# Performance work log

Measured on AMD Instinct MI355X. Metric: run time of the kernel, lower is better.

The kernel has to match this reference:

```python
import jax, jax.numpy as jnp
import numpy as np

B, S, E, H = 16, 2048, 512, 64


def setup_inputs() -> dict:
    key = jax.random.key(0)
    k1, k2, k3, k4, k5 = jax.random.split(key, 5)
    inp = {
        "input": jax.random.normal(k1, (B, S, E), dtype=jnp.float32),
        "seq_lengths": jax.random.randint(k2, (B,), 0, S).astype(jnp.int64),
        "Wq": jax.random.normal(k3, (E, H), dtype=jnp.float32) * (1.0 / np.sqrt(E)),
        "Wk": jax.random.normal(k4, (E, H), dtype=jnp.float32) * (1.0 / np.sqrt(E)),
        "Wv": jax.random.normal(k5, (E, H), dtype=jnp.float32) * (1.0 / np.sqrt(E)),
    }
    return inp


def reference(input, seq_lengths, Wq, Wk, Wv):
    # Projections (bias-free Linear): [B,S,E] @ [E,H] -> [B,S,H]
    q = input @ Wq
    k = input @ Wk
    v = input @ Wv
    Sdim = input.shape[1]
    head_size = Wk.shape[-1]
    # Padding mask: position >= seq_length -> True. Zero out q and k (NOT v),
    # exactly as the torch module does with masked_fill.
    pad = (jnp.arange(Sdim)[None, :] >= seq_lengths[:, None])[:, :, None]  # [B,S,1]
    q = jnp.where(pad, 0.0, q)
    k = jnp.where(pad, 0.0, k)
    scale = 1.0 / np.sqrt(head_size).astype(np.float32)
    # Full score matrix [B,S,S] (the memory-bound intermediate)
    scores = jnp.einsum("bsh,bth->bst", q, k) * scale
    weights = jax.nn.softmax(scores, axis=-1)
    weights = jnp.where(jnp.isnan(weights), 0.0, weights)
    out = jnp.einsum("bst,bth->bsh", weights, v)  # [B,S,H]
    return out
```

## Files before the change

kernel.cpp:

```cpp
#include <hip/hip_runtime.h>
#include <hip/hip_bf16.h>

typedef __bf16 bf16;
typedef __bf16 bf16x8 __attribute__((ext_vector_type(8)));
typedef __bf16 bf16x4 __attribute__((ext_vector_type(4)));
typedef float  f32x4  __attribute__((ext_vector_type(4)));

static constexpr int SDIM = 2048;
static constexpr int EDIM = 512;
static constexpr int HDIM = 64;

typedef __attribute__((address_space(1))) const void* gptr_t;
typedef __attribute__((address_space(3))) void*       lptr_t;

__device__ __forceinline__ void gl_lds16(const bf16* g, bf16* l) {
  __builtin_amdgcn_global_load_lds((gptr_t)g, (lptr_t)l, 16, 0, 0);
}

#if __has_builtin(__builtin_amdgcn_exp2f)
#define EXP2F(x) __builtin_amdgcn_exp2f(x)
#else
#define EXP2F(x) exp2f(x)
#endif

__device__ __forceinline__ bf16x8 pack8(f32x4 a, f32x4 b) {
  bf16x8 r;
  r[0] = (bf16)a[0]; r[1] = (bf16)a[1]; r[2] = (bf16)a[2]; r[3] = (bf16)a[3];
  r[4] = (bf16)b[0]; r[5] = (bf16)b[1]; r[6] = (bf16)b[2]; r[7] = (bf16)b[3];
  return r;
}

__global__ __launch_bounds__(256) void wt_kernel(const float* __restrict__ Wq,
                                                 const float* __restrict__ Wk,
                                                 const float* __restrict__ Wv,
                                                 bf16* __restrict__ Wt) {
  __shared__ float lds[64][65];
  const int mat = blockIdx.x >> 3;
  const int et  = blockIdx.x & 7;
  const float* W = (mat == 0) ? Wq : ((mat == 1) ? Wk : Wv);
  const float scale = (mat == 0) ? 0.18033688f : 1.0f;
  const int t  = threadIdx.x;
  const int er = t >> 2;
  const int c4 = (t & 3) * 16;
#pragma unroll
  for (int j = 0; j < 4; ++j) {
    f32x4 v = *(const f32x4*)(W + (size_t)(et * 64 + er) * HDIM + c4 + j * 4);
    lds[er][c4 + j * 4 + 0] = v[0]; lds[er][c4 + j * 4 + 1] = v[1];
    lds[er][c4 + j * 4 + 2] = v[2]; lds[er][c4 + j * 4 + 3] = v[3];
  }
  __syncthreads();
  const int h  = t >> 2;
  const int ec = (t & 3) * 16;
  bf16x8 o0, o1;
#pragma unroll
  for (int j = 0; j < 8; ++j) o0[j] = (bf16)(lds[ec + j][h] * scale);
#pragma unroll
  for (int j = 0; j < 8; ++j) o1[j] = (bf16)(lds[ec + 8 + j][h] * scale);
  bf16* dst = Wt + mat * (HDIM * EDIM) + (size_t)h * EDIM + et * 64 + ec;
  *(bf16x8*)dst = o0;
  *(bf16x8*)(dst + 8) = o1;
}

__global__ __launch_bounds__(256) void proj_kernel(const float* __restrict__ x,
                                                   const bf16* __restrict__ Wt,
                                                   const int* __restrict__ lens,
                                                   bf16* __restrict__ qo,
                                                   bf16* __restrict__ ko,
                                                   bf16* __restrict__ vT) {
  __shared__ __align__(16) bf16 wbuf[2][192 * 64];
  const int tid  = threadIdx.x;
  const int wave = tid >> 6;
  const int lane = tid & 63;
  const int quad = lane >> 4;
  const int l16  = lane & 15;
  const int rowbase = blockIdx.x * 64 + wave * 16;
  const int b = blockIdx.x >> 5;
  const float* xrow = x + (size_t)(rowbase + l16) * EDIM + quad * 8;
  const int srow   = lane >> 3;
  const int schunk = (lane & 7) ^ srow;

  #define WSTAGE(ck, buf) { _Pragma("unroll")                                  \
    for (int i6 = 0; i6 < 6; ++i6) {                                           \
      const int R0 = (wave * 6 + i6) * 8;                                      \
      gl_lds16(Wt + (size_t)(R0 + srow) * EDIM + (ck) * 64 + schunk * 8,       \
               &(buf)[R0 * 64]); } }

  f32x4 acc[3][4];
#pragma unroll
  for (int m = 0; m < 3; ++m)
#pragma unroll
    for (int nt = 0; nt < 4; ++nt) acc[m][nt] = (f32x4){0.f, 0.f, 0.f, 0.f};

  #define WCOMPUTE(buf, eo4, afrag) { _Pragma("unroll")                        \
    for (int m = 0; m < 3; ++m) { _Pragma("unroll")                            \
      for (int nt = 0; nt < 4; ++nt) {                                         \
        bf16x8 bfv = *(const bf16x8*)(&(buf)[(m * 64 + nt * 16 + l16) * 64 +   \
                                             ((((eo4) + quad) ^ (l16 & 7)) * 8)]); \
        acc[m][nt] = __builtin_amdgcn_mfma_f32_16x16x32_bf16(afrag, bfv, acc[m][nt], 0, 0, 0); } } }

  WSTAGE(0, wbuf[0]);
  f32x4 xA0 = *(const f32x4*)(xrow);
  f32x4 xB0 = *(const f32x4*)(xrow + 4);
  f32x4 xA1 = *(const f32x4*)(xrow + 32);
  f32x4 xB1 = *(const f32x4*)(xrow + 36);
#pragma unroll 2
  for (int ck = 0; ck < 8; ++ck) {
    __syncthreads();
    const int ksn = (ck < 7) ? (ck + 1) * 2 : 14;
    f32x4 nA0 = *(const f32x4*)(xrow + ksn * 32);
    f32x4 nB0 = *(const f32x4*)(xrow + ksn * 32 + 4);
    f32x4 nA1 = *(const f32x4*)(xrow + ksn * 32 + 32);
    f32x4 nB1 = *(const f32x4*)(xrow + ksn * 32 + 36);
    if (ck + 1 < 8) WSTAGE(ck + 1, wbuf[(ck + 1) & 1]);
    bf16x8 a = pack8(xA0, xB0);
    WCOMPUTE(wbuf[ck & 1], 0, a);
    a = pack8(xA1, xB1);
    WCOMPUTE(wbuf[ck & 1], 4, a);
    xA0 = nA0; xB0 = nB0; xA1 = nA1; xB1 = nB1;
  }

  int odd_or = 0;
#pragma unroll
  for (int i = 1; i < 16; i += 2) odd_or |= lens[i];
  const int len = (odd_or == 0) ? lens[2 * b] : lens[b];

#pragma unroll
  for (int nt = 0; nt < 4; ++nt) {
    const int h = nt * 16 + l16;
    bf16x4 vv;
#pragma unroll
    for (int r = 0; r < 4; ++r) {
      const int row = rowbase + quad * 4 + r;
      const int s = row & (SDIM - 1);
      const bool pad = (s >= len);
      qo[(size_t)row * HDIM + h] = (bf16)(pad ? 0.f : acc[0][nt][r]);
      ko[(size_t)row * HDIM + h] = (bf16)(pad ? 0.f : acc[1][nt][r]);
      vv[r] = (bf16)acc[2][nt][r];
    }
    *(bf16x4*)(vT + ((size_t)b * HDIM + h) * SDIM + (rowbase & (SDIM - 1)) + quad * 4) = vv;
  }
  #undef WSTAGE
  #undef WCOMPUTE
}

__global__ __launch_bounds__(256) void attn_kernel(const bf16* __restrict__ qb,
                                                   const bf16* __restrict__ kb,
                                                   const bf16* __restrict__ vT,
                                                   float* __restrict__ out) {
  __shared__ __align__(16) bf16 Kbuf[2][64 * 64];
  __shared__ __align__(16) bf16 Vbuf[2][64 * 64];
  __shared__ __align__(16) bf16 plds[4][2][16 * 64];
  const int tid  = threadIdx.x;
  const int wave = tid >> 6;
  const int lane = tid & 63;
  const int quad = lane >> 4;
  const int l16  = lane & 15;
  const int xcd = blockIdx.x & 7;
  const int jj  = blockIdx.x >> 3;
  const int b   = xcd * 2 + (jj >> 5);
  const int qbase = (jj & 31) * 64 + wave * 16;
  const bf16* q0 = qb + (size_t)b * SDIM * HDIM;
  const bf16* k0 = kb + (size_t)b * SDIM * HDIM;
  const bf16* v0 = vT + (size_t)b * HDIM * SDIM;
  const int swz = (l16 & 7) << 3;
  const int srow   = lane >> 3;
  const int schunk = (lane & 7) ^ (srow & 7);

  bf16x8 qf[2];
#pragma unroll
  for (int c = 0; c < 2; ++c)
    qf[c] = *(const bf16x8*)(q0 + (size_t)(qbase + l16) * HDIM + c * 32 + quad * 8);

  f32x4 O[4];
  float l_acc = 0.f;
#pragma unroll
  for (int ht = 0; ht < 4; ++ht) O[ht] = (f32x4){0.f, 0.f, 0.f, 0.f};
  bf16x8 vfp[4][2];

  #define STAGE(sidx, KB, VB)                                                  \
    {                                                                          \
      const int key0_ = (sidx) * 64;                                           \
      _Pragma("unroll")                                                        \
      for (int j8 = 0; j8 < 2; ++j8) {                                         \
        const int r0 = wave * 16 + j8 * 8;                                     \
        gl_lds16(k0 + (size_t)(key0_ + r0 + srow) * HDIM + schunk * 8,         \
                 &(KB)[r0 * 64]);                                              \
        gl_lds16(v0 + (size_t)(r0 + srow) * SDIM + key0_ + schunk * 8,         \
                 &(VB)[r0 * 64]);                                              \
      }                                                                        \
    }

  STAGE(0, Kbuf[0], Vbuf[0]);
#pragma unroll 2
  for (int s = 0; s < 32; ++s) {
    __syncthreads();
    if (s + 1 < 32) STAGE(s + 1, Kbuf[(s + 1) & 1], Vbuf[(s + 1) & 1]);
    const bf16* KB = Kbuf[s & 1];
    const bf16* VB = Vbuf[s & 1];
    bf16* PW = &plds[wave][s & 1][0];
    const bf16* PR = &plds[wave][(s & 1) ^ 1][0];

    bf16x8 pa[2];
    if (s) {
#pragma unroll
      for (int kc = 0; kc < 2; ++kc)
        pa[kc] = *(const bf16x8*)(&PR[l16 * 64 + (((kc * 4 + quad) << 3) ^ swz)]);
    }

    bf16x8 kf[4][2], vf[4][2];
#pragma unroll
    for (int kt = 0; kt < 4; ++kt)
#pragma unroll
      for (int c = 0; c < 2; ++c)
        kf[kt][c] = *(const bf16x8*)(&KB[(kt * 16 + l16) * 64 + (((c * 4 + quad) << 3) ^ swz)]);
#pragma unroll
    for (int ht = 0; ht < 4; ++ht)
#pragma unroll
      for (int kc = 0; kc < 2; ++kc)
        vf[ht][kc] = *(const bf16x8*)(&VB[(ht * 16 + l16) * 64 + (((kc * 4 + quad) << 3) ^ swz)]);

#pragma unroll
    for (int kt = 0; kt < 4; ++kt) {
      f32x4 st = (f32x4){0.f, 0.f, 0.f, 0.f};
      st = __builtin_amdgcn_mfma_f32_16x16x32_bf16(kf[kt][0], qf[0], st, 0, 0, 0);
      st = __builtin_amdgcn_mfma_f32_16x16x32_bf16(kf[kt][1], qf[1], st, 0, 0, 0);
      f32x4 p;
      p[0] = EXP2F(st[0]); p[1] = EXP2F(st[1]);
      p[2] = EXP2F(st[2]); p[3] = EXP2F(st[3]);
      l_acc += (p[0] + p[1]) + (p[2] + p[3]);
      bf16x4 pb;
      pb[0] = (bf16)p[0]; pb[1] = (bf16)p[1]; pb[2] = (bf16)p[2]; pb[3] = (bf16)p[3];
      const int coff = (((kt * 2 + (quad >> 1)) << 3) ^ swz) + (quad & 1) * 4;
      *(bf16x4*)(&PW[l16 * 64 + coff]) = pb;
    }

    if (s) {
#pragma unroll
      for (int ht = 0; ht < 4; ++ht) {
        O[ht] = __builtin_amdgcn_mfma_f32_16x16x32_bf16(pa[0], vfp[ht][0], O[ht], 0, 0, 0);
        O[ht] = __builtin_amdgcn_mfma_f32_16x16x32_bf16(pa[1], vfp[ht][1], O[ht], 0, 0, 0);
      }
    }
#pragma unroll
    for (int ht = 0; ht < 4; ++ht)
#pragma unroll
      for (int kc = 0; kc < 2; ++kc) vfp[ht][kc] = vf[ht][kc];
  }

  {
    bf16x8 pa[2];
    const bf16* PR = &plds[wave][1][0];
#pragma unroll
    for (int kc = 0; kc < 2; ++kc)
      pa[kc] = *(const bf16x8*)(&PR[l16 * 64 + (((kc * 4 + quad) << 3) ^ swz)]);
#pragma unroll
    for (int ht = 0; ht < 4; ++ht) {
      O[ht] = __builtin_amdgcn_mfma_f32_16x16x32_bf16(pa[0], vfp[ht][0], O[ht], 0, 0, 0);
      O[ht] = __builtin_amdgcn_mfma_f32_16x16x32_bf16(pa[1], vfp[ht][1], O[ht], 0, 0, 0);
    }
  }

  l_acc += __shfl_xor(l_acc, 16);
  l_acc += __shfl_xor(l_acc, 32);
  const float inv_own = 1.0f / l_acc;
#pragma unroll
  for (int r = 0; r < 4; ++r) {
    const float inv = __shfl(inv_own, (lane & 48) + quad * 4 + r);
    const int row = qbase + quad * 4 + r;
#pragma unroll
    for (int ht = 0; ht < 4; ++ht)
      out[((size_t)b * SDIM + row) * HDIM + ht * 16 + l16] = O[ht][r] * inv;
  }
  #undef STAGE
}

extern "C" void kernel_launch(void* const* d_in, const int* in_sizes, int n_in,
                              void* d_out, int out_size, void* d_ws, size_t ws_size,
                              hipStream_t stream) {
  (void)in_sizes; (void)n_in; (void)out_size; (void)ws_size;
  const float* x  = (const float*)d_in[0];
  const int*   sl = (const int*)d_in[1];
  const float* Wq = (const float*)d_in[2];
  const float* Wk = (const float*)d_in[3];
  const float* Wv = (const float*)d_in[4];
  float* out = (float*)d_out;

  char* ws = (char*)d_ws;
  bf16* Wt = (bf16*)(ws);
  bf16* qb = (bf16*)(ws + (256 << 10));
  bf16* kb = (bf16*)(ws + (256 << 10) + (4 << 20));
  bf16* vT = (bf16*)(ws + (256 << 10) + (8 << 20));

  wt_kernel  <<<24,  256, 0, stream>>>(Wq, Wk, Wv, Wt);
  proj_kernel<<<512, 256, 0, stream>>>(x, Wt, sl, qb, kb, vT);
  attn_kernel<<<512, 256, 0, stream>>>(qb, kb, vT, out);
}
```

Baseline: 141.3 us.

## Load V fragments directly from global into registers instead of via LDS

Removes the LDS staging buffer for V. Each wave now loads its V MFMA operand fragments straight from global memory into a double-buffered register array one step ahead, and the P·V MFMA is moved to the start of each iteration. This cuts LDS traffic and footprint, which could raise occupancy. The cost is that every wave redundantly loads the same V tile from global/L2, and register pressure rises.

```diff
diff --git a/kernel.cpp b/kernel.cpp
--- a/kernel.cpp
+++ b/kernel.cpp
@@ -148,7 +148,6 @@
                                                    const bf16* __restrict__ vT,
                                                    float* __restrict__ out) {
   __shared__ __align__(16) bf16 Kbuf[2][64 * 64];
-  __shared__ __align__(16) bf16 Vbuf[2][64 * 64];
   __shared__ __align__(16) bf16 plds[4][2][16 * 64];
   const int tid  = threadIdx.x;
   const int wave = tid >> 6;
@@ -175,9 +174,8 @@
   float l_acc = 0.f;
 #pragma unroll
   for (int ht = 0; ht < 4; ++ht) O[ht] = (f32x4){0.f, 0.f, 0.f, 0.f};
-  bf16x8 vfp[4][2];
-
-  #define STAGE(sidx, KB, VB)                                                  \
+
+  #define STAGEK(sidx, KB)                                                     \
     {                                                                          \
       const int key0_ = (sidx) * 64;                                           \
       _Pragma("unroll")                                                        \
@@ -185,39 +183,50 @@
         const int r0 = wave * 16 + j8 * 8;                                     \
         gl_lds16(k0 + (size_t)(key0_ + r0 + srow) * HDIM + schunk * 8,         \
                  &(KB)[r0 * 64]);                                              \
-        gl_lds16(v0 + (size_t)(r0 + srow) * SDIM + key0_ + schunk * 8,         \
-                 &(VB)[r0 * 64]);                                              \
       }                                                                        \
     }
 
-  STAGE(0, Kbuf[0], Vbuf[0]);
+  #define VLOAD(sidx, dst)                                                     \
+    {                                                                          \
+      const int key0_ = (sidx) * 64;                                           \
+      _Pragma("unroll")                                                        \
+      for (int ht = 0; ht < 4; ++ht)                                           \
+        _Pragma("unroll")                                                      \
+        for (int kc = 0; kc < 2; ++kc)                                         \
+          dst[ht][kc] = *(const bf16x8*)(v0 + (size_t)(ht * 16 + l16) * SDIM + \
+                                         key0_ + kc * 32 + quad * 8);          \
+    }
+
+  bf16x8 vv[2][4][2];
+  STAGEK(0, Kbuf[0]);
+  VLOAD(0, vv[0]);
 #pragma unroll 2
   for (int s = 0; s < 32; ++s) {
     __syncthreads();
-    if (s + 1 < 32) STAGE(s + 1, Kbuf[(s + 1) & 1], Vbuf[(s + 1) & 1]);
+    if (s + 1 < 32) STAGEK(s + 1, Kbuf[(s + 1) & 1]);
     const bf16* KB = Kbuf[s & 1];
-    const bf16* VB = Vbuf[s & 1];
     bf16* PW = &plds[wave][s & 1][0];
     const bf16* PR = &plds[wave][(s & 1) ^ 1][0];
 
-    bf16x8 pa[2];
     if (s) {
+      bf16x8 pa[2];
 #pragma unroll
       for (int kc = 0; kc < 2; ++kc)
         pa[kc] = *(const bf16x8*)(&PR[l16 * 64 + (((kc * 4 + quad) << 3) ^ swz)]);
-    }
-
-    bf16x8 kf[4][2], vf[4][2];
+#pragma unroll
+      for (int ht = 0; ht < 4; ++ht) {
+        O[ht] = __builtin_amdgcn_mfma_f32_16x16x32_bf16(pa[0], vv[(s - 1) & 1][ht][0], O[ht], 0, 0, 0);
+        O[ht] = __builtin_amdgcn_mfma_f32_16x16x32_bf16(pa[1], vv[(s - 1) & 1][ht][1], O[ht], 0, 0, 0);
+      }
+    }
+    if (s + 1 < 32) VLOAD(s + 1, vv[(s + 1) & 1]);
+
+    bf16x8 kf[4][2];
 #pragma unroll
     for (int kt = 0; kt < 4; ++kt)
 #pragma unroll
       for (int c = 0; c < 2; ++c)
         kf[kt][c] = *(const bf16x8*)(&KB[(kt * 16 + l16) * 64 + (((c * 4 + quad) << 3) ^ swz)]);
-#pragma unroll
-    for (int ht = 0; ht < 4; ++ht)
-#pragma unroll
-      for (int kc = 0; kc < 2; ++kc)
-        vf[ht][kc] = *(const bf16x8*)(&VB[(ht * 16 + l16) * 64 + (((kc * 4 + quad) << 3) ^ swz)]);
 
 #pragma unroll
     for (int kt = 0; kt < 4; ++kt) {
@@ -233,21 +242,10 @@
       const int coff = (((kt * 2 + (quad >> 1)) << 3) ^ swz) + (quad & 1) * 4;
       *(bf16x4*)(&PW[l16 * 64 + coff]) = pb;
     }
-
-    if (s) {
-#pragma unroll
-      for (int ht = 0; ht < 4; ++ht) {
-        O[ht] = __builtin_amdgcn_mfma_f32_16x16x32_bf16(pa[0], vfp[ht][0], O[ht], 0, 0, 0);
-        O[ht] = __builtin_amdgcn_mfma_f32_16x16x32_bf16(pa[1], vfp[ht][1], O[ht], 0, 0, 0);
-      }
-    }
-#pragma unroll
-    for (int ht = 0; ht < 4; ++ht)
-#pragma unroll
-      for (int kc = 0; kc < 2; ++kc) vfp[ht][kc] = vf[ht][kc];
   }
 
   {
+    __builtin_amdgcn_s_waitcnt(0xc07f);
     bf16x8 pa[2];
     const bf16* PR = &plds[wave][1][0];
 #pragma unroll
@@ -255,8 +253,8 @@
       pa[kc] = *(const bf16x8*)(&PR[l16 * 64 + (((kc * 4 + quad) << 3) ^ swz)]);
 #pragma unroll
     for (int ht = 0; ht < 4; ++ht) {
-      O[ht] = __builtin_amdgcn_mfma_f32_16x16x32_bf16(pa[0], vfp[ht][0], O[ht], 0, 0, 0);
-      O[ht] = __builtin_amdgcn_mfma_f32_16x16x32_bf16(pa[1], vfp[ht][1], O[ht], 0, 0, 0);
+      O[ht] = __builtin_amdgcn_mfma_f32_16x16x32_bf16(pa[0], vv[1][ht][0], O[ht], 0, 0, 0);
+      O[ht] = __builtin_amdgcn_mfma_f32_16x16x32_bf16(pa[1], vv[1][ht][1], O[ht], 0, 0, 0);
     }
   }
 
@@ -271,7 +269,8 @@
     for (int ht = 0; ht < 4; ++ht)
       out[((size_t)b * SDIM + row) * HDIM + ht * 16 + l16] = O[ht][r] * inv;
   }
-  #undef STAGE
+  #undef STAGEK
+  #undef VLOAD
 }
 
 extern "C" void kernel_launch(void* const* d_in, const int* in_sizes, int n_in,
```

Measured after the change: 173.4 us. 22.7% more time.
